# Optimization experiments

Measured on AMD Instinct MI355X. Metric: run time of the kernel, lower is better.

Reference implementation:

```python
import jax, jax.numpy as jnp
import numpy as np

B, S, D = 8, 160, 256


def setup_inputs() -> dict:
    key = jax.random.key(0)
    kx, kw, kb = jax.random.split(key, 3)
    x = jax.random.normal(kx, (B, S, D), dtype=jnp.float32)
    # torch nn.Linear(2D, D): weight [D, 2D], bias [D]; store transposed W [2D, D]
    lim = 1.0 / np.sqrt(2 * D)
    W = jax.random.uniform(kw, (2 * D, D), minval=-lim, maxval=lim, dtype=jnp.float32)
    b = jax.random.uniform(kb, (D,), minval=-lim, maxval=lim, dtype=jnp.float32)
    return {"x": x, "W": W, "b": b}


def reference(x, W, b):
    Bsz, Ssz, Dsz = x.shape
    # all i<j pairs in the same order as the nested python loop (i outer, j inner)
    idx_i, idx_j = jnp.triu_indices(Ssz, k=1)  # each [P], P = S(S-1)/2
    # fc_rel(cat(x_i, x_j)) = x_i @ W[:D] + x_j @ W[D:] + b
    Wi, Wj = W[:Dsz], W[Dsz:]
    xa = jnp.einsum('bsd,de->bse', x, Wi)  # [B,S,D]
    xb = jnp.einsum('bsd,de->bse', x, Wj)  # [B,S,D]
    return xa[:, idx_i, :] + xb[:, idx_j, :] + b  # [B,P,D]
```

## Files before the change

### kernel.cpp

```cpp
#include <hip/hip_runtime.h>

#define SS 160
#define DD 256
#define BB 8
#define NPAIR 12720
#define M_TOT (BB * SS)

__global__ __launch_bounds__(256) void gemm_kernel(const float* __restrict__ x,
                                                   const float* __restrict__ W,
                                                   const float* __restrict__ bias,
                                                   float* __restrict__ y) {
    const int BM = 32, BN = 64, BK = 32;
    __shared__ float As[BK][BM + 1];
    __shared__ float Bs[BK][BN];

    const int n0 = blockIdx.x * BN;
    const int m0 = blockIdx.y * BM;
    const int half = (n0 >= DD) ? 1 : 0;
    const float* Wbase = W + (half ? DD * DD : 0);
    const int ncol0 = n0 - (half ? DD : 0);

    const int tid = threadIdx.x;
    const int tx = tid & 15;
    const int ty = tid >> 4;

    const int ar = tid >> 3;
    const int ac = (tid & 7) << 2;
    const int bkr = tid >> 4;
    const int bnc = (tid & 15) << 2;

    float acc0[4] = {0.f, 0.f, 0.f, 0.f};
    float acc1[4] = {0.f, 0.f, 0.f, 0.f};

    for (int k0 = 0; k0 < DD; k0 += BK) {
        float4 av = *(const float4*)(x + (m0 + ar) * DD + k0 + ac);
        float4 b0 = *(const float4*)(Wbase + (k0 + bkr) * DD + ncol0 + bnc);
        float4 b1 = *(const float4*)(Wbase + (k0 + bkr + 16) * DD + ncol0 + bnc);
        __syncthreads();
        As[ac + 0][ar] = av.x;
        As[ac + 1][ar] = av.y;
        As[ac + 2][ar] = av.z;
        As[ac + 3][ar] = av.w;
        *(float4*)(&Bs[bkr][bnc])      = b0;
        *(float4*)(&Bs[bkr + 16][bnc]) = b1;
        __syncthreads();
#pragma unroll
        for (int kk = 0; kk < BK; ++kk) {
            float a0 = As[kk][ty];
            float a1 = As[kk][ty + 16];
            float4 bv = *(const float4*)(&Bs[kk][tx << 2]);
            acc0[0] += a0 * bv.x; acc0[1] += a0 * bv.y;
            acc0[2] += a0 * bv.z; acc0[3] += a0 * bv.w;
            acc1[0] += a1 * bv.x; acc1[1] += a1 * bv.y;
            acc1[2] += a1 * bv.z; acc1[3] += a1 * bv.w;
        }
    }

    float4 bias4 = make_float4(0.f, 0.f, 0.f, 0.f);
    if (!half) bias4 = *(const float4*)(bias + ncol0 + (tx << 2));

    float* yout = y + (half ? M_TOT * DD : 0);
    float4 r0, r1;
    r0.x = acc0[0] + bias4.x; r0.y = acc0[1] + bias4.y;
    r0.z = acc0[2] + bias4.z; r0.w = acc0[3] + bias4.w;
    r1.x = acc1[0] + bias4.x; r1.y = acc1[1] + bias4.y;
    r1.z = acc1[2] + bias4.z; r1.w = acc1[3] + bias4.w;
    *(float4*)(yout + (m0 + ty) * DD + ncol0 + (tx << 2))      = r0;
    *(float4*)(yout + (m0 + ty + 16) * DD + ncol0 + (tx << 2)) = r1;
}

__global__ __launch_bounds__(256) void expand_kernel(const float* __restrict__ y,
                                                     float* __restrict__ out) {
    const int row  = (blockIdx.x << 2) + (threadIdx.x >> 6);
    const int lane = threadIdx.x & 63;
    const unsigned b = (unsigned)row / NPAIR;
    const int p = row - (int)b * NPAIR;

    float disc = sqrtf((float)(101761 - 8 * p));
    int i = (int)((319.0f - disc) * 0.5f);
    if (i < 0) i = 0;
    if (i > SS - 2) i = SS - 2;
    while (i > 0 && (i * (2 * SS - 1 - i)) / 2 > p) --i;
    while (((i + 1) * (2 * SS - 2 - i)) / 2 <= p) ++i;
    const int j = i + 1 + p - (i * (2 * SS - 1 - i)) / 2;

    const float4* ya = (const float4*)y;
    const float4* yb = (const float4*)(y + M_TOT * DD);
    float4 va = ya[(((int)b * SS + i) << 6) + lane];
    float4 vb = yb[(((int)b * SS + j) << 6) + lane];
    float4 r;
    r.x = va.x + vb.x; r.y = va.y + vb.y;
    r.z = va.z + vb.z; r.w = va.w + vb.w;
    ((float4*)out)[(row << 6) + lane] = r;
}

extern "C" void kernel_launch(void* const* d_in, const int* in_sizes, int n_in,
                              void* d_out, int out_size, void* d_ws, size_t ws_size,
                              hipStream_t stream) {
    const float* x    = (const float*)d_in[0];
    const float* W    = (const float*)d_in[1];
    const float* bias = (const float*)d_in[2];
    float* y   = (float*)d_ws;
    float* out = (float*)d_out;

    dim3 gemm_grid(512 / 64, 1280 / 32);
    gemm_kernel<<<gemm_grid, 256, 0, stream>>>(x, W, bias, y);

    const int rows = BB * NPAIR;
    expand_kernel<<<rows / 4, 256, 0, stream>>>(y, out);
}
```

Baseline: 136.9 us.

## Enlarge GEMM tile to 4x4 micro-tiles and index expand kernel by row i

The GEMM now uses a 64x64 block tile in which each thread computes a 4x4 micro-tile with float4 reads from shared memory, which raises arithmetic intensity and halves the number of GEMM blocks. The expand kernel now assigns one block per (i, batch) pair, loads the xa row once, and loops over every j>i. This removes the per-row sqrt-based pair index decode. The grid becomes uneven, since i=0 blocks do 159 rows and late blocks do very few, and the smaller GEMM grid (160 blocks) may underfill the GPU.

Result: faster. 129.9 us (-5.1%).

```diff
diff --git a/kernel.cpp b/kernel.cpp
--- a/kernel.cpp
+++ b/kernel.cpp
@@ -10,8 +10,8 @@
                                                    const float* __restrict__ W,
                                                    const float* __restrict__ bias,
                                                    float* __restrict__ y) {
-    const int BM = 32, BN = 64, BK = 32;
-    __shared__ float As[BK][BM + 1];
+    const int BM = 64, BN = 64, BK = 32;
+    __shared__ float As[BK][BM + 4];
     __shared__ float Bs[BK][BN];
 
     const int n0 = blockIdx.x * BN;
@@ -24,35 +24,40 @@
     const int tx = tid & 15;
     const int ty = tid >> 4;
 
-    const int ar = tid >> 3;
-    const int ac = (tid & 7) << 2;
-    const int bkr = tid >> 4;
-    const int bnc = (tid & 15) << 2;
+    const int ar = tid & 63;
+    const int ak = (tid >> 6) << 3;
+    const int bk = tid >> 3;
+    const int bc = (tid & 7) << 3;
 
-    float acc0[4] = {0.f, 0.f, 0.f, 0.f};
-    float acc1[4] = {0.f, 0.f, 0.f, 0.f};
+    float4 acc[4];
+#pragma unroll
+    for (int r = 0; r < 4; ++r) acc[r] = make_float4(0.f, 0.f, 0.f, 0.f);
 
     for (int k0 = 0; k0 < DD; k0 += BK) {
-        float4 av = *(const float4*)(x + (m0 + ar) * DD + k0 + ac);
-        float4 b0 = *(const float4*)(Wbase + (k0 + bkr) * DD + ncol0 + bnc);
-        float4 b1 = *(const float4*)(Wbase + (k0 + bkr + 16) * DD + ncol0 + bnc);
+        float4 a0 = *(const float4*)(x + (m0 + ar) * DD + k0 + ak);
+        float4 a1 = *(const float4*)(x + (m0 + ar) * DD + k0 + ak + 4);
+        float4 b0 = *(const float4*)(Wbase + (k0 + bk) * DD + ncol0 + bc);
+        float4 b1 = *(const float4*)(Wbase + (k0 + bk) * DD + ncol0 + bc + 4);
         __syncthreads();
-        As[ac + 0][ar] = av.x;
-        As[ac + 1][ar] = av.y;
-        As[ac + 2][ar] = av.z;
-        As[ac + 3][ar] = av.w;
-        *(float4*)(&Bs[bkr][bnc])      = b0;
-        *(float4*)(&Bs[bkr + 16][bnc]) = b1;
+        As[ak + 0][ar] = a0.x; As[ak + 1][ar] = a0.y;
+        As[ak + 2][ar] = a0.z; As[ak + 3][ar] = a0.w;
+        As[ak + 4][ar] = a1.x; As[ak + 5][ar] = a1.y;
+        As[ak + 6][ar] = a1.z; As[ak + 7][ar] = a1.w;
+        *(float4*)(&Bs[bk][bc])     = b0;
+        *(float4*)(&Bs[bk][bc + 4]) = b1;
         __syncthreads();
 #pragma unroll
         for (int kk = 0; kk < BK; ++kk) {
-            float a0 = As[kk][ty];
-            float a1 = As[kk][ty + 16];
+            float4 av = *(const float4*)(&As[kk][ty << 2]);
             float4 bv = *(const float4*)(&Bs[kk][tx << 2]);
-            acc0[0] += a0 * bv.x; acc0[1] += a0 * bv.y;
-            acc0[2] += a0 * bv.z; acc0[3] += a0 * bv.w;
-            acc1[0] += a1 * bv.x; acc1[1] += a1 * bv.y;
-            acc1[2] += a1 * bv.z; acc1[3] += a1 * bv.w;
+            acc[0].x += av.x * bv.x; acc[0].y += av.x * bv.y;
+            acc[0].z += av.x * bv.z; acc[0].w += av.x * bv.w;
+            acc[1].x += av.y * bv.x; acc[1].y += av.y * bv.y;
+            acc[1].z += av.y * bv.z; acc[1].w += av.y * bv.w;
+            acc[2].x += av.z * bv.x; acc[2].y += av.z * bv.y;
+            acc[2].z += av.z * bv.z; acc[2].w += av.z * bv.w;
+            acc[3].x += av.w * bv.x; acc[3].y += av.w * bv.y;
+            acc[3].z += av.w * bv.z; acc[3].w += av.w * bv.w;
         }
     }
 
@@ -60,38 +65,38 @@
     if (!half) bias4 = *(const float4*)(bias + ncol0 + (tx << 2));
 
     float* yout = y + (half ? M_TOT * DD : 0);
-    float4 r0, r1;
-    r0.x = acc0[0] + bias4.x; r0.y = acc0[1] + bias4.y;
-    r0.z = acc0[2] + bias4.z; r0.w = acc0[3] + bias4.w;
-    r1.x = acc1[0] + bias4.x; r1.y = acc1[1] + bias4.y;
-    r1.z = acc1[2] + bias4.z; r1.w = acc1[3] + bias4.w;
-    *(float4*)(yout + (m0 + ty) * DD + ncol0 + (tx << 2))      = r0;
-    *(float4*)(yout + (m0 + ty + 16) * DD + ncol0 + (tx << 2)) = r1;
+#pragma unroll
+    for (int r = 0; r < 4; ++r) {
+        float4 v;
+        v.x = acc[r].x + bias4.x; v.y = acc[r].y + bias4.y;
+        v.z = acc[r].z + bias4.z; v.w = acc[r].w + bias4.w;
+        *(float4*)(yout + (m0 + (ty << 2) + r) * DD + ncol0 + (tx << 2)) = v;
+    }
 }
 
 __global__ __launch_bounds__(256) void expand_kernel(const float* __restrict__ y,
                                                      float* __restrict__ out) {
-    const int row  = (blockIdx.x << 2) + (threadIdx.x >> 6);
+    const int i = blockIdx.x;
+    const int b = blockIdx.y;
+    const int w = threadIdx.x >> 6;
     const int lane = threadIdx.x & 63;
-    const unsigned b = (unsigned)row / NPAIR;
-    const int p = row - (int)b * NPAIR;
-
-    float disc = sqrtf((float)(101761 - 8 * p));
-    int i = (int)((319.0f - disc) * 0.5f);
-    if (i < 0) i = 0;
-    if (i > SS - 2) i = SS - 2;
-    while (i > 0 && (i * (2 * SS - 1 - i)) / 2 > p) --i;
-    while (((i + 1) * (2 * SS - 2 - i)) / 2 <= p) ++i;
-    const int j = i + 1 + p - (i * (2 * SS - 1 - i)) / 2;
+    const int L = SS - 1 - i;
 
     const float4* ya = (const float4*)y;
     const float4* yb = (const float4*)(y + M_TOT * DD);
-    float4 va = ya[(((int)b * SS + i) << 6) + lane];
-    float4 vb = yb[(((int)b * SS + j) << 6) + lane];
-    float4 r;
-    r.x = va.x + vb.x; r.y = va.y + vb.y;
-    r.z = va.z + vb.z; r.w = va.w + vb.w;
-    ((float4*)out)[(row << 6) + lane] = r;
+    const float4 va = ya[((b * SS + i) << 6) + lane];
+
+    const float4* ybb = yb + (((b * SS + i + 1) << 6) + lane);
+    float4* ob = (float4*)out + (((b * NPAIR + (i * (2 * SS - 1 - i)) / 2) << 6) + lane);
+
+#pragma unroll 4
+    for (int r = w; r < L; r += 4) {
+        float4 vb = ybb[r << 6];
+        float4 o;
+        o.x = va.x + vb.x; o.y = va.y + vb.y;
+        o.z = va.z + vb.z; o.w = va.w + vb.w;
+        ob[r << 6] = o;
+    }
 }
 
 extern "C" void kernel_launch(void* const* d_in, const int* in_sizes, int n_in,
@@ -103,9 +108,9 @@
     float* y   = (float*)d_ws;
     float* out = (float*)d_out;
 
-    dim3 gemm_grid(512 / 64, 1280 / 32);
+    dim3 gemm_grid(512 / 64, 1280 / 64);
     gemm_kernel<<<gemm_grid, 256, 0, stream>>>(x, W, bias, y);
 
-    const int rows = BB * NPAIR;
-    expand_kernel<<<rows / 4, 256, 0, stream>>>(y, out);
+    dim3 exp_grid(SS - 1, BB);
+    expand_kernel<<<exp_grid, 256, 0, stream>>>(y, out);
 }
```
